# Kernel tuning notes

Measured on AMD Instinct MI355X. Metric: run time of the kernel, lower is better.

The kernel has to match this reference:

```python
import jax, jax.numpy as jnp
import numpy as np

B, S, H, NH = 2, 2048, 2048, 16
HD = H // NH
CLIP_QKV = 8.0
SOFTMAX_SCALE = 1.0 / np.sqrt(HD)
NEG_INF = jnp.finfo(jnp.float32).min


def setup_inputs() -> dict:
    key = jax.random.key(0)
    k1, k2, k3, k4 = jax.random.split(key, 4)
    hidden_states = jax.random.normal(k1, (B, S, H), dtype=jnp.float32)
    position_bias = jax.random.normal(k2, (NH, S, S), dtype=jnp.float32) * 0.1
    # causal mask: True = masked out (upper triangle)
    causal = ~jnp.tril(jnp.ones((S, S), dtype=bool))
    attention_mask = jnp.broadcast_to(causal[None, None], (B, 1, S, S))
    Wqkv = jax.random.normal(k3, (3 * H, H), dtype=jnp.float32) * (1.0 / np.sqrt(H))
    Wout = jax.random.normal(k4, (H, H), dtype=jnp.float32) * (1.0 / np.sqrt(H))
    return {"hidden_states": hidden_states, "position_bias": position_bias,
            "attention_mask": attention_mask, "Wqkv": Wqkv, "Wout": Wout}


def reference(hidden_states, position_bias, attention_mask, Wqkv, Wout):
    # QKV projection (no bias) + clamp
    mixed = hidden_states @ Wqkv.T                        # [B,S,3H]
    mixed = jnp.clip(mixed, -CLIP_QKV, CLIP_QKV)
    q, k, v = jnp.split(mixed, 3, axis=2)
    # [B,S,H] -> [B,NH,S,HD]
    def split_heads(x):
        return x.reshape(B, S, NH, HD).transpose(0, 2, 1, 3)
    q, k, v = split_heads(q), split_heads(k), split_heads(v)
    scores = jnp.einsum('bhqd,bhkd->bhqk', q, k) * SOFTMAX_SCALE
    # full position bias is used (slicing indices are always 0 in source)
    scores = scores + position_bias[None]                 # [B,NH,S,S]
    scores = jnp.where(attention_mask, NEG_INF, scores)
    attn = jax.nn.softmax(scores.astype(jnp.float32), axis=-1).astype(v.dtype)
    ctx = jnp.einsum('bhqk,bhkd->bhqd', attn, v)          # [B,NH,S,HD]
    ctx = ctx.transpose(0, 2, 1, 3).reshape(B, S, H)
    attn_output = ctx @ Wout.T
    return attn_output
```

## Files before the change

### kernel.cpp

```cpp
#include <hip/hip_runtime.h>
#include <hip/hip_bf16.h>
#include <stdint.h>

typedef __bf16 bf16x8 __attribute__((ext_vector_type(8)));
typedef float f32x4 __attribute__((ext_vector_type(4)));

#define SOFTMAX_SCALE 0.08838834764831845f
#define LOG2E 1.44269504088896f

__device__ __forceinline__ bf16x8 load8_cvt(const __hip_bfloat16* p) {
  return *(const bf16x8*)p;
}
__device__ __forceinline__ bf16x8 load8_cvt(const float* p) {
  float4 a = *(const float4*)p;
  float4 b = *(const float4*)(p + 4);
  bf16x8 r;
  r[0] = (__bf16)a.x; r[1] = (__bf16)a.y; r[2] = (__bf16)a.z; r[3] = (__bf16)a.w;
  r[4] = (__bf16)b.x; r[5] = (__bf16)b.y; r[6] = (__bf16)b.z; r[7] = (__bf16)b.w;
  return r;
}

__device__ __forceinline__ void gload_lds16(const __hip_bfloat16* g,
                                            __hip_bfloat16* l) {
  __builtin_amdgcn_global_load_lds(
      (__attribute__((address_space(1))) void*)(g),
      (__attribute__((address_space(3))) void*)(l), 16, 0, 0);
}

__global__ __launch_bounds__(256) void cvt_f32_bf16(
    const float* __restrict__ in, __hip_bfloat16* __restrict__ out, int n8)
{
  int i = blockIdx.x * blockDim.x + threadIdx.x;
  int stride = gridDim.x * blockDim.x;
  for (; i < n8; i += stride)
    *(bf16x8*)(out + (int64_t)i * 8) = load8_cvt(in + (int64_t)i * 8);
}

template <typename TA, typename TB>
__device__ __forceinline__ void gemm_bt_loop(
    const TA* __restrict__ A,
    const TB* __restrict__ B,
    int K, int m0, int n0,
    __hip_bfloat16* As, __hip_bfloat16* Bs,
    f32x4 acc[4][4])
{
  const int t = threadIdx.x;
  const int w = t >> 6, lane = t & 63;
  const int wm = (w >> 1) * 64, wn = (w & 1) * 64;
  const int l16 = lane & 15, quad = lane >> 4;
  constexpr bool ASYNC = (sizeof(TA) == 2) && (sizeof(TB) == 2);

  for (int k0 = 0; k0 < K; k0 += 64) {
    if constexpr (ASYNC) {
      #pragma unroll
      for (int i = 0; i < 4; ++i) {
        int cb = (w * 4 + i) * 64;
        int idx = cb + lane;
        int row = idx >> 3;
        int chs = (idx & 7) ^ (row & 7);
        gload_lds16((const __hip_bfloat16*)A + (int64_t)(m0 + row) * K + k0 + chs * 8,
                    As + cb * 8);
        gload_lds16((const __hip_bfloat16*)B + (int64_t)(n0 + row) * K + k0 + chs * 8,
                    Bs + cb * 8);
      }
    } else {
      #pragma unroll
      for (int i = 0; i < 4; ++i) {
        int idx = i * 256 + t;
        int row = idx >> 3, ch = idx & 7;
        int sw = (ch ^ (row & 7)) * 8;
        *(bf16x8*)(As + row * 64 + sw) =
            load8_cvt(A + (int64_t)(m0 + row) * K + k0 + ch * 8);
        *(bf16x8*)(Bs + row * 64 + sw) =
            load8_cvt(B + (int64_t)(n0 + row) * K + k0 + ch * 8);
      }
    }
    __syncthreads();
    #pragma unroll
    for (int ks = 0; ks < 2; ++ks) {
      bf16x8 af[4], bfr[4];
      #pragma unroll
      for (int mt = 0; mt < 4; ++mt) {
        int row = wm + mt * 16 + l16;
        int ch = ks * 4 + quad;
        af[mt] = *(const bf16x8*)(As + row * 64 + ((ch ^ (row & 7)) * 8));
      }
      #pragma unroll
      for (int nt = 0; nt < 4; ++nt) {
        int row = wn + nt * 16 + l16;
        int ch = ks * 4 + quad;
        bfr[nt] = *(const bf16x8*)(Bs + row * 64 + ((ch ^ (row & 7)) * 8));
      }
      #pragma unroll
      for (int mt = 0; mt < 4; ++mt)
        #pragma unroll
        for (int nt = 0; nt < 4; ++nt)
          acc[mt][nt] = __builtin_amdgcn_mfma_f32_16x16x32_bf16(
              af[mt], bfr[nt], acc[mt][nt], 0, 0, 0);
    }
    __syncthreads();
  }
}

template <typename TA, typename TB>
__global__ __launch_bounds__(256) void qkv_gemm(
    const TA* __restrict__ A,
    const TB* __restrict__ W,
    __hip_bfloat16* __restrict__ qb,
    __hip_bfloat16* __restrict__ kb,
    __hip_bfloat16* __restrict__ vb)
{
  __shared__ __align__(16) __hip_bfloat16 As[128 * 64];
  __shared__ __align__(16) __hip_bfloat16 Bs[128 * 64];
  const f32x4 z4 = {0.f, 0.f, 0.f, 0.f};
  f32x4 acc[4][4];
  #pragma unroll
  for (int mt = 0; mt < 4; ++mt)
    #pragma unroll
    for (int nt = 0; nt < 4; ++nt) acc[mt][nt] = z4;

  const int K = 2048;
  const int n0 = blockIdx.x * 128, m0 = blockIdx.y * 128;
  gemm_bt_loop(A, W, K, m0, n0, As, Bs, acc);

  const int t = threadIdx.x;
  const int w = t >> 6, lane = t & 63;
  const int wm = (w >> 1) * 64, wn = (w & 1) * 64;
  const int l16 = lane & 15, quad = lane >> 4;
  __hip_bfloat16* bufs[3] = {qb, kb, vb};
  #pragma unroll
  for (int nt = 0; nt < 4; ++nt) {
    int gn = n0 + wn + nt * 16 + l16;
    int which = gn >> 11;
    int hc = gn & 2047;
    int head = hc >> 7, d = hc & 127;
    __hip_bfloat16* dst = bufs[which];
    #pragma unroll
    for (int mt = 0; mt < 4; ++mt) {
      #pragma unroll
      for (int r = 0; r < 4; ++r) {
        int gm = m0 + wm + mt * 16 + quad * 4 + r;
        int bb = gm >> 11, s = gm & 2047;
        float val = acc[mt][nt][r];
        val = fminf(8.f, fmaxf(-8.f, val));
        dst[(((int64_t)(bb * 16 + head) * 2048 + s) << 7) + d] =
            __float2bfloat16(val);
      }
    }
  }
}

__global__ __launch_bounds__(256) void transpose_v(
    const __hip_bfloat16* __restrict__ V,
    __hip_bfloat16* __restrict__ Vt)
{
  __shared__ __hip_bfloat16 tile[64][68];
  const int bh = blockIdx.z;
  const int s0 = blockIdx.x * 64;
  const int d0 = blockIdx.y * 64;
  const int t = threadIdx.x;
  const int c = t & 63, rq = t >> 6;
  const __hip_bfloat16* Vp = V + (int64_t)bh * 2048 * 128;
  #pragma unroll
  for (int j = 0; j < 16; ++j) {
    int r = rq * 16 + j;
    tile[r][c] = Vp[(int64_t)(s0 + r) * 128 + d0 + c];
  }
  __syncthreads();
  __hip_bfloat16* Vo = Vt + (int64_t)bh * 128 * 2048;
  #pragma unroll
  for (int j = 0; j < 16; ++j) {
    int dd = rq * 16 + j;
    Vo[(int64_t)(d0 + dd) * 2048 + s0 + c] = tile[c][dd];
  }
}

__global__ __launch_bounds__(256, 2) void attn_kernel(
    const __hip_bfloat16* __restrict__ Q,
    const __hip_bfloat16* __restrict__ Kg,
    const __hip_bfloat16* __restrict__ Vt,
    const float* __restrict__ bias,
    __hip_bfloat16* __restrict__ ctx)
{
  __shared__ __align__(16) __hip_bfloat16 Ks[128 * 128];
  __shared__ __align__(16) __hip_bfloat16 Vs[128 * 128];
  __shared__ __align__(16) __hip_bfloat16 Bs[64 * 128];

  const int t = threadIdx.x;
  const int w = t >> 6, lane = t & 63;
  const int l16 = lane & 15, quad = lane >> 4;

  const int bh = blockIdx.y;
  const int h = bh & 15, b = bh >> 4;
  const int qt = 31 - (int)blockIdx.x;
  const int q0 = qt * 64;

  bf16x8 qf[4];
  {
    const __hip_bfloat16* Qp = Q + ((int64_t)bh * 2048 + q0 + w * 16) * 128;
    #pragma unroll
    for (int ks = 0; ks < 4; ++ks)
      qf[ks] = *(const bf16x8*)(Qp + l16 * 128 + ks * 32 + quad * 8);
  }

  const f32x4 z4 = {0.f, 0.f, 0.f, 0.f};
  f32x4 O[8];
  #pragma unroll
  for (int nt = 0; nt < 8; ++nt) O[nt] = z4;
  float m_r[4], l_r[4];
  #pragma unroll
  for (int r = 0; r < 4; ++r) { m_r[r] = -3.0e38f; l_r[r] = 0.f; }

  const __hip_bfloat16* Kbase = Kg + (int64_t)bh * 2048 * 128;
  const __hip_bfloat16* Vbase = Vt + (int64_t)bh * 128 * 2048;
  const float* Bbase = bias + (int64_t)h * 2048 * 2048;

  const int ktmax = qt >> 1;
  for (int kt = 0; kt <= ktmax; ++kt) {
    const __hip_bfloat16* Kp = Kbase + (int64_t)kt * 128 * 128;
    const __hip_bfloat16* Vp = Vbase + kt * 128;
    #pragma unroll
    for (int i = 0; i < 8; ++i) {
      int cb = (w * 8 + i) * 64;
      int idx = cb + lane;
      int row = idx >> 4;
      int chs = (idx & 15) ^ (row & 15);
      gload_lds16(Kp + row * 128 + chs * 8, Ks + cb * 8);
      gload_lds16(Vp + (int64_t)row * 2048 + chs * 8, Vs + cb * 8);
    }
    #pragma unroll
    for (int i = 0; i < 4; ++i) {
      int idx = i * 256 + t;
      int brow = idx >> 4, ch = idx & 15;
      int sw = (ch ^ (brow & 15)) * 8;
      *(bf16x8*)(Bs + brow * 128 + sw) =
          load8_cvt(Bbase + (int64_t)(q0 + brow) * 2048 + kt * 128 + ch * 8);
    }
    __syncthreads();

    f32x4 S[8];
    #pragma unroll
    for (int nt = 0; nt < 8; ++nt) S[nt] = z4;
    #pragma unroll
    for (int ks = 0; ks < 4; ++ks) {
      bf16x8 kf[8];
      #pragma unroll
      for (int nt = 0; nt < 8; ++nt) {
        int row = nt * 16 + l16;
        int ch = ks * 4 + quad;
        kf[nt] = *(const bf16x8*)(Ks + row * 128 + ((ch ^ (row & 15)) * 8));
      }
      #pragma unroll
      for (int nt = 0; nt < 8; ++nt)
        S[nt] = __builtin_amdgcn_mfma_f32_16x16x32_bf16(
            qf[ks], kf[nt], S[nt], 0, 0, 0);
    }

    const bool diag = (kt == ktmax);
    #pragma unroll
    for (int r = 0; r < 4; ++r) {
      int trow = w * 16 + quad * 4 + r;
      int gq = q0 + trow;
      #pragma unroll
      for (int nt = 0; nt < 8; ++nt) {
        int col = nt * 16 + l16;
        float bv = __bfloat162float(
            Bs[trow * 128 + (((col >> 3) ^ (trow & 15)) << 3) + (col & 7)]);
        float sv = S[nt][r] * SOFTMAX_SCALE + bv;
        if (diag && (kt * 128 + col > gq)) sv = -3.0e38f;
        S[nt][r] = sv;
      }
    }

    #pragma unroll
    for (int r = 0; r < 4; ++r) {
      float rm = S[0][r];
      #pragma unroll
      for (int nt = 1; nt < 8; ++nt) rm = fmaxf(rm, S[nt][r]);
      rm = fmaxf(rm, __shfl_xor(rm, 1, 64));
      rm = fmaxf(rm, __shfl_xor(rm, 2, 64));
      rm = fmaxf(rm, __shfl_xor(rm, 4, 64));
      rm = fmaxf(rm, __shfl_xor(rm, 8, 64));
      float mo = m_r[r];
      float mn = fmaxf(mo, rm);
      float alpha = exp2f((mo - mn) * LOG2E);
      float rs = 0.f;
      #pragma unroll
      for (int nt = 0; nt < 8; ++nt) {
        float pv = exp2f((S[nt][r] - mn) * LOG2E);
        S[nt][r] = pv;
        rs += pv;
      }
      rs += __shfl_xor(rs, 1, 64);
      rs += __shfl_xor(rs, 2, 64);
      rs += __shfl_xor(rs, 4, 64);
      rs += __shfl_xor(rs, 8, 64);
      m_r[r] = mn;
      l_r[r] = l_r[r] * alpha + rs;
      #pragma unroll
      for (int nt = 0; nt < 8; ++nt) O[nt][r] *= alpha;
    }
    __syncthreads();

    #pragma unroll
    for (int r = 0; r < 4; ++r) {
      int trow = w * 16 + quad * 4 + r;
      #pragma unroll
      for (int nt = 0; nt < 8; ++nt) {
        int col = nt * 16 + l16;
        Bs[trow * 128 + (((col >> 3) ^ (trow & 15)) << 3) + (col & 7)] =
            __float2bfloat16(S[nt][r]);
      }
    }
    __syncthreads();

    #pragma unroll
    for (int ksp = 0; ksp < 4; ++ksp) {
      int ch = ksp * 4 + quad;
      int prow = w * 16 + l16;
      bf16x8 pf = *(const bf16x8*)(Bs + prow * 128 + ((ch ^ (prow & 15)) * 8));
      bf16x8 vf[8];
      #pragma unroll
      for (int nt = 0; nt < 8; ++nt) {
        int row = nt * 16 + l16;
        vf[nt] = *(const bf16x8*)(Vs + row * 128 + ((ch ^ (row & 15)) * 8));
      }
      #pragma unroll
      for (int nt = 0; nt < 8; ++nt)
        O[nt] = __builtin_amdgcn_mfma_f32_16x16x32_bf16(
            pf, vf[nt], O[nt], 0, 0, 0);
    }
    __syncthreads();
  }

  #pragma unroll
  for (int r = 0; r < 4; ++r) {
    int trow = w * 16 + quad * 4 + r;
    int gm = b * 2048 + q0 + trow;
    float inv = 1.f / l_r[r];
    __hip_bfloat16* crow = ctx + (int64_t)gm * 2048 + h * 128;
    #pragma unroll
    for (int nt = 0; nt < 8; ++nt)
      crow[nt * 16 + l16] = __float2bfloat16(O[nt][r] * inv);
  }
}

template <typename TB>
__global__ __launch_bounds__(256) void out_gemm(
    const __hip_bfloat16* __restrict__ A,
    const TB* __restrict__ W,
    float* __restrict__ out)
{
  __shared__ __align__(16) __hip_bfloat16 As[128 * 64];
  __shared__ __align__(16) __hip_bfloat16 Bs[128 * 64];
  const f32x4 z4 = {0.f, 0.f, 0.f, 0.f};
  f32x4 acc[4][4];
  #pragma unroll
  for (int mt = 0; mt < 4; ++mt)
    #pragma unroll
    for (int nt = 0; nt < 4; ++nt) acc[mt][nt] = z4;

  const int K = 2048;
  const int n0 = blockIdx.x * 128, m0 = blockIdx.y * 128;
  gemm_bt_loop(A, W, K, m0, n0, As, Bs, acc);

  const int t = threadIdx.x;
  const int w = t >> 6, lane = t & 63;
  const int wm = (w >> 1) * 64, wn = (w & 1) * 64;
  const int l16 = lane & 15, quad = lane >> 4;
  #pragma unroll
  for (int mt = 0; mt < 4; ++mt) {
    #pragma unroll
    for (int r = 0; r < 4; ++r) {
      int gm = m0 + wm + mt * 16 + quad * 4 + r;
      #pragma unroll
      for (int nt = 0; nt < 4; ++nt) {
        int gn = n0 + wn + nt * 16 + l16;
        out[(int64_t)gm * 2048 + gn] = acc[mt][nt][r];
      }
    }
  }
}

extern "C" void kernel_launch(void* const* d_in, const int* in_sizes, int n_in,
                              void* d_out, int out_size, void* d_ws, size_t ws_size,
                              hipStream_t stream) {
  const float* hs   = (const float*)d_in[0];
  const float* bias = (const float*)d_in[1];
  const float* Wqkv = (const float*)d_in[3];
  const float* Wout = (const float*)d_in[4];
  float* out = (float*)d_out;

  __hip_bfloat16* ws = (__hip_bfloat16*)d_ws;
  const size_t SEG = (size_t)32 * 2048 * 128;
  __hip_bfloat16* q   = ws;
  __hip_bfloat16* k   = ws + SEG;
  __hip_bfloat16* v   = ws + 2 * SEG;
  __hip_bfloat16* vt  = ws + 3 * SEG;
  __hip_bfloat16* ctx = ws + 2 * SEG;

  const size_t NW_QKV = (size_t)6144 * 2048;
  const size_t NW_OUT = (size_t)2048 * 2048;
  const size_t need_bytes = (4 * SEG + NW_QKV + SEG) * sizeof(__hip_bfloat16);

  if (ws_size >= need_bytes) {
    __hip_bfloat16* wqkvb = ws + 4 * SEG;
    __hip_bfloat16* hsb   = wqkvb + NW_QKV;
    __hip_bfloat16* woutb = wqkvb;
    cvt_f32_bf16<<<1024, 256, 0, stream>>>(hs, hsb, (int)(SEG / 8));
    cvt_f32_bf16<<<1024, 256, 0, stream>>>(Wqkv, wqkvb, (int)(NW_QKV / 8));
    qkv_gemm<__hip_bfloat16, __hip_bfloat16>
        <<<dim3(48, 32), 256, 0, stream>>>(hsb, wqkvb, q, k, v);
    transpose_v<<<dim3(32, 2, 32), 256, 0, stream>>>(v, vt);
    cvt_f32_bf16<<<1024, 256, 0, stream>>>(Wout, woutb, (int)(NW_OUT / 8));
    attn_kernel<<<dim3(32, 32), 256, 0, stream>>>(q, k, vt, bias, ctx);
    out_gemm<__hip_bfloat16><<<dim3(16, 32), 256, 0, stream>>>(ctx, woutb, out);
  } else {
    qkv_gemm<float, float><<<dim3(48, 32), 256, 0, stream>>>(hs, Wqkv, q, k, v);
    transpose_v<<<dim3(32, 2, 32), 256, 0, stream>>>(v, vt);
    attn_kernel<<<dim3(32, 32), 256, 0, stream>>>(q, k, vt, bias, ctx);
    out_gemm<float><<<dim3(16, 32), 256, 0, stream>>>(ctx, Wout, out);
  }
}
```

Before: 740.8 us.

## Double-buffer K/V tiles with 64-key steps and register-prefetched bias

Restructures the attention inner loop to process 64-key tiles with double-buffered K and V in LDS. The next tile is prefetched through global_load_lds while the current one is computed, using manual vmcnt waits and raw barriers. Bias is now loaded straight into registers one step ahead instead of being staged through LDS, and MFMA sections get raised wave priority. The grid mapping is also changed to interleave batch and head. The cost is more loop iterations, smaller MFMA batches per step, and fragile hand-written waitcnt counts.

```diff
diff --git a/kernel.cpp b/kernel.cpp
--- a/kernel.cpp
+++ b/kernel.cpp
@@ -175,6 +175,134 @@
   }
 }
 
+__device__ __forceinline__ void attn_step(
+    int kt, int ktmax, int q0,
+    const __hip_bfloat16* Kbase, const __hip_bfloat16* Vbase, const float* Bb,
+    __hip_bfloat16* Kcur, __hip_bfloat16* Vcur,
+    __hip_bfloat16* Knxt, __hip_bfloat16* Vnxt,
+    __hip_bfloat16* Ps,
+    const bf16x8 (&qf)[4],
+    float (&bcur)[16], float (&bnxt)[16],
+    f32x4 (&O)[8], float (&m_r)[4], float (&l_r)[4],
+    int w, int lane, int l16, int quad)
+{
+  if (kt < ktmax) {
+    const __hip_bfloat16* Kp = Kbase + (int64_t)(kt + 1) * 64 * 128;
+    const __hip_bfloat16* Vp = Vbase + (kt + 1) * 64;
+    #pragma unroll
+    for (int i = 0; i < 4; ++i) {
+      int cb = (w * 4 + i) * 64;
+      int idx = cb + lane;
+      { int row = idx >> 4, chs = (idx & 15) ^ (row & 15);
+        gload_lds16(Kp + row * 128 + chs * 8, Knxt + cb * 8); }
+      { int row = idx >> 3, chs = (idx & 7) ^ (row & 7);
+        gload_lds16(Vp + (int64_t)row * 2048 + chs * 8, Vnxt + cb * 8); }
+    }
+    const float* bp = Bb + (int64_t)(q0 + w * 16 + quad * 4) * 2048
+                      + (kt + 1) * 64 + l16;
+    #pragma unroll
+    for (int nt = 0; nt < 4; ++nt)
+      #pragma unroll
+      for (int r = 0; r < 4; ++r)
+        bnxt[nt * 4 + r] = bp[(int64_t)r * 2048 + nt * 16];
+    asm volatile("s_waitcnt vmcnt(24)" ::: "memory");
+  } else {
+    asm volatile("s_waitcnt vmcnt(0)" ::: "memory");
+  }
+  __builtin_amdgcn_s_barrier();
+
+  const f32x4 z4 = {0.f, 0.f, 0.f, 0.f};
+  f32x4 S[4];
+  #pragma unroll
+  for (int nt = 0; nt < 4; ++nt) S[nt] = z4;
+  __builtin_amdgcn_s_setprio(1);
+  #pragma unroll
+  for (int ks = 0; ks < 4; ++ks) {
+    int ch = ks * 4 + quad;
+    bf16x8 kf[4];
+    #pragma unroll
+    for (int nt = 0; nt < 4; ++nt) {
+      int row = nt * 16 + l16;
+      kf[nt] = *(const bf16x8*)(Kcur + row * 128 + ((ch ^ (row & 15)) * 8));
+    }
+    #pragma unroll
+    for (int nt = 0; nt < 4; ++nt)
+      S[nt] = __builtin_amdgcn_mfma_f32_16x16x32_bf16(
+          qf[ks], kf[nt], S[nt], 0, 0, 0);
+  }
+  __builtin_amdgcn_s_setprio(0);
+
+  const bool diag = (kt == ktmax);
+  #pragma unroll
+  for (int r = 0; r < 4; ++r) {
+    int trow = w * 16 + quad * 4 + r;
+    int gq = q0 + trow;
+    #pragma unroll
+    for (int nt = 0; nt < 4; ++nt) {
+      int col = kt * 64 + nt * 16 + l16;
+      float sv = S[nt][r] * SOFTMAX_SCALE + bcur[nt * 4 + r];
+      if (diag && col > gq) sv = -3.0e38f;
+      S[nt][r] = sv;
+    }
+  }
+
+  #pragma unroll
+  for (int r = 0; r < 4; ++r) {
+    float rm = fmaxf(fmaxf(S[0][r], S[1][r]), fmaxf(S[2][r], S[3][r]));
+    rm = fmaxf(rm, __shfl_xor(rm, 1, 64));
+    rm = fmaxf(rm, __shfl_xor(rm, 2, 64));
+    rm = fmaxf(rm, __shfl_xor(rm, 4, 64));
+    rm = fmaxf(rm, __shfl_xor(rm, 8, 64));
+    float mo = m_r[r];
+    float mn = fmaxf(mo, rm);
+    float alpha = exp2f((mo - mn) * LOG2E);
+    float rs = 0.f;
+    #pragma unroll
+    for (int nt = 0; nt < 4; ++nt) {
+      float pv = exp2f((S[nt][r] - mn) * LOG2E);
+      S[nt][r] = pv;
+      rs += pv;
+    }
+    rs += __shfl_xor(rs, 1, 64);
+    rs += __shfl_xor(rs, 2, 64);
+    rs += __shfl_xor(rs, 4, 64);
+    rs += __shfl_xor(rs, 8, 64);
+    m_r[r] = mn;
+    l_r[r] = l_r[r] * alpha + rs;
+    #pragma unroll
+    for (int nt2 = 0; nt2 < 8; ++nt2) O[nt2][r] *= alpha;
+  }
+
+  #pragma unroll
+  for (int r = 0; r < 4; ++r) {
+    int trow = w * 16 + quad * 4 + r;
+    #pragma unroll
+    for (int nt = 0; nt < 4; ++nt) {
+      int col = nt * 16 + l16;
+      Ps[trow * 64 + (((col >> 3) ^ (trow & 7)) << 3) + (col & 7)] =
+          __float2bfloat16(S[nt][r]);
+    }
+  }
+
+  __builtin_amdgcn_s_setprio(1);
+  #pragma unroll
+  for (int ksp = 0; ksp < 2; ++ksp) {
+    int ch = ksp * 4 + quad;
+    int prow = w * 16 + l16;
+    bf16x8 pf = *(const bf16x8*)(Ps + prow * 64 + ((ch ^ (prow & 7)) * 8));
+    #pragma unroll
+    for (int nt = 0; nt < 8; ++nt) {
+      int row = nt * 16 + l16;
+      bf16x8 vf = *(const bf16x8*)(Vcur + row * 64 + ((ch ^ (row & 7)) * 8));
+      O[nt] = __builtin_amdgcn_mfma_f32_16x16x32_bf16(pf, vf, O[nt], 0, 0, 0);
+    }
+  }
+  __builtin_amdgcn_s_setprio(0);
+
+  asm volatile("s_waitcnt lgkmcnt(0)" ::: "memory");
+  __builtin_amdgcn_s_barrier();
+}
+
 __global__ __launch_bounds__(256, 2) void attn_kernel(
     const __hip_bfloat16* __restrict__ Q,
     const __hip_bfloat16* __restrict__ Kg,
@@ -182,18 +310,20 @@
     const float* __restrict__ bias,
     __hip_bfloat16* __restrict__ ctx)
 {
-  __shared__ __align__(16) __hip_bfloat16 Ks[128 * 128];
-  __shared__ __align__(16) __hip_bfloat16 Vs[128 * 128];
-  __shared__ __align__(16) __hip_bfloat16 Bs[64 * 128];
+  __shared__ __align__(16) __hip_bfloat16 KsBuf[2][64 * 128];
+  __shared__ __align__(16) __hip_bfloat16 VsBuf[2][128 * 64];
+  __shared__ __align__(16) __hip_bfloat16 Ps[64 * 64];
 
   const int t = threadIdx.x;
   const int w = t >> 6, lane = t & 63;
   const int l16 = lane & 15, quad = lane >> 4;
 
-  const int bh = blockIdx.y;
-  const int h = bh & 15, b = bh >> 4;
+  const int y = blockIdx.y;
+  const int h = y >> 1, b = y & 1;
+  const int bh = b * 16 + h;
   const int qt = 31 - (int)blockIdx.x;
   const int q0 = qt * 64;
+  const int ktmax = qt;
 
   bf16x8 qf[4];
   {
@@ -213,124 +343,36 @@
 
   const __hip_bfloat16* Kbase = Kg + (int64_t)bh * 2048 * 128;
   const __hip_bfloat16* Vbase = Vt + (int64_t)bh * 128 * 2048;
-  const float* Bbase = bias + (int64_t)h * 2048 * 2048;
-
-  const int ktmax = qt >> 1;
-  for (int kt = 0; kt <= ktmax; ++kt) {
-    const __hip_bfloat16* Kp = Kbase + (int64_t)kt * 128 * 128;
-    const __hip_bfloat16* Vp = Vbase + kt * 128;
-    #pragma unroll
-    for (int i = 0; i < 8; ++i) {
-      int cb = (w * 8 + i) * 64;
+  const float* Bb = bias + (int64_t)h * 2048 * 2048;
+
+  float bA[16], bB[16];
+
+  {
+    #pragma unroll
+    for (int i = 0; i < 4; ++i) {
+      int cb = (w * 4 + i) * 64;
       int idx = cb + lane;
-      int row = idx >> 4;
-      int chs = (idx & 15) ^ (row & 15);
-      gload_lds16(Kp + row * 128 + chs * 8, Ks + cb * 8);
-      gload_lds16(Vp + (int64_t)row * 2048 + chs * 8, Vs + cb * 8);
-    }
-    #pragma unroll
-    for (int i = 0; i < 4; ++i) {
-      int idx = i * 256 + t;
-      int brow = idx >> 4, ch = idx & 15;
-      int sw = (ch ^ (brow & 15)) * 8;
-      *(bf16x8*)(Bs + brow * 128 + sw) =
-          load8_cvt(Bbase + (int64_t)(q0 + brow) * 2048 + kt * 128 + ch * 8);
-    }
-    __syncthreads();
-
-    f32x4 S[8];
-    #pragma unroll
-    for (int nt = 0; nt < 8; ++nt) S[nt] = z4;
-    #pragma unroll
-    for (int ks = 0; ks < 4; ++ks) {
-      bf16x8 kf[8];
-      #pragma unroll
-      for (int nt = 0; nt < 8; ++nt) {
-        int row = nt * 16 + l16;
-        int ch = ks * 4 + quad;
-        kf[nt] = *(const bf16x8*)(Ks + row * 128 + ((ch ^ (row & 15)) * 8));
-      }
-      #pragma unroll
-      for (int nt = 0; nt < 8; ++nt)
-        S[nt] = __builtin_amdgcn_mfma_f32_16x16x32_bf16(
-            qf[ks], kf[nt], S[nt], 0, 0, 0);
-    }
-
-    const bool diag = (kt == ktmax);
-    #pragma unroll
-    for (int r = 0; r < 4; ++r) {
-      int trow = w * 16 + quad * 4 + r;
-      int gq = q0 + trow;
-      #pragma unroll
-      for (int nt = 0; nt < 8; ++nt) {
-        int col = nt * 16 + l16;
-        float bv = __bfloat162float(
-            Bs[trow * 128 + (((col >> 3) ^ (trow & 15)) << 3) + (col & 7)]);
-        float sv = S[nt][r] * SOFTMAX_SCALE + bv;
-        if (diag && (kt * 128 + col > gq)) sv = -3.0e38f;
-        S[nt][r] = sv;
-      }
-    }
-
-    #pragma unroll
-    for (int r = 0; r < 4; ++r) {
-      float rm = S[0][r];
-      #pragma unroll
-      for (int nt = 1; nt < 8; ++nt) rm = fmaxf(rm, S[nt][r]);
-      rm = fmaxf(rm, __shfl_xor(rm, 1, 64));
-      rm = fmaxf(rm, __shfl_xor(rm, 2, 64));
-      rm = fmaxf(rm, __shfl_xor(rm, 4, 64));
-      rm = fmaxf(rm, __shfl_xor(rm, 8, 64));
-      float mo = m_r[r];
-      float mn = fmaxf(mo, rm);
-      float alpha = exp2f((mo - mn) * LOG2E);
-      float rs = 0.f;
-      #pragma unroll
-      for (int nt = 0; nt < 8; ++nt) {
-        float pv = exp2f((S[nt][r] - mn) * LOG2E);
-        S[nt][r] = pv;
-        rs += pv;
-      }
-      rs += __shfl_xor(rs, 1, 64);
-      rs += __shfl_xor(rs, 2, 64);
-      rs += __shfl_xor(rs, 4, 64);
-      rs += __shfl_xor(rs, 8, 64);
-      m_r[r] = mn;
-      l_r[r] = l_r[r] * alpha + rs;
-      #pragma unroll
-      for (int nt = 0; nt < 8; ++nt) O[nt][r] *= alpha;
-    }
-    __syncthreads();
-
-    #pragma unroll
-    for (int r = 0; r < 4; ++r) {
-      int trow = w * 16 + quad * 4 + r;
-      #pragma unroll
-      for (int nt = 0; nt < 8; ++nt) {
-        int col = nt * 16 + l16;
-        Bs[trow * 128 + (((col >> 3) ^ (trow & 15)) << 3) + (col & 7)] =
-            __float2bfloat16(S[nt][r]);
-      }
-    }
-    __syncthreads();
-
-    #pragma unroll
-    for (int ksp = 0; ksp < 4; ++ksp) {
-      int ch = ksp * 4 + quad;
-      int prow = w * 16 + l16;
-      bf16x8 pf = *(const bf16x8*)(Bs + prow * 128 + ((ch ^ (prow & 15)) * 8));
-      bf16x8 vf[8];
-      #pragma unroll
-      for (int nt = 0; nt < 8; ++nt) {
-        int row = nt * 16 + l16;
-        vf[nt] = *(const bf16x8*)(Vs + row * 128 + ((ch ^ (row & 15)) * 8));
-      }
-      #pragma unroll
-      for (int nt = 0; nt < 8; ++nt)
-        O[nt] = __builtin_amdgcn_mfma_f32_16x16x32_bf16(
-            pf, vf[nt], O[nt], 0, 0, 0);
-    }
-    __syncthreads();
+      { int row = idx >> 4, chs = (idx & 15) ^ (row & 15);
+        gload_lds16(Kbase + row * 128 + chs * 8, KsBuf[0] + cb * 8); }
+      { int row = idx >> 3, chs = (idx & 7) ^ (row & 7);
+        gload_lds16(Vbase + (int64_t)row * 2048 + chs * 8, VsBuf[0] + cb * 8); }
+    }
+    const float* bp = Bb + (int64_t)(q0 + w * 16 + quad * 4) * 2048 + l16;
+    #pragma unroll
+    for (int nt = 0; nt < 4; ++nt)
+      #pragma unroll
+      for (int r = 0; r < 4; ++r)
+        bA[nt * 4 + r] = bp[(int64_t)r * 2048 + nt * 16];
+  }
+
+  for (int kt = 0; kt <= ktmax; kt += 2) {
+    attn_step(kt, ktmax, q0, Kbase, Vbase, Bb,
+              KsBuf[0], VsBuf[0], KsBuf[1], VsBuf[1], Ps, qf,
+              bA, bB, O, m_r, l_r, w, lane, l16, quad);
+    if (kt + 1 <= ktmax)
+      attn_step(kt + 1, ktmax, q0, Kbase, Vbase, Bb,
+                KsBuf[1], VsBuf[1], KsBuf[0], VsBuf[0], Ps, qf,
+                bB, bA, O, m_r, l_r, w, lane, l16, quad);
   }
 
   #pragma unroll
```

Result: no change. 748.1 us (+1.0%).
